# Performance work log

Hardware: AMD Instinct MI355X
Metric: run time of the kernel (lower is better)

Reference implementation:

```python
import jax, jax.numpy as jnp
from jax import lax
import numpy as np

DN = ('NDHWC', 'DHWIO', 'NDHWC')

def conv3d(x, w, b, stride=1):
    return lax.conv_general_dilated(x, w, (stride,) * 3, 'SAME', dimension_numbers=DN) + b

def convT3d(x, w, b, stride=2):
    return lax.conv_transpose(x, w, (stride,) * 3, 'SAME', dimension_numbers=DN) + b

def prelu(x, a):
    return jnp.where(x > 0, x, a * x)

def bn(x, g, be, m, v):
    # keras BatchNormalization, inference mode, epsilon=1e-3
    return (x - m) * g * lax.rsqrt(v + 1e-3) + be

def res_unit(x, c1w, c1b, c2w, c2b, g, be, m, v, a):
    # VQVAEResidualUnit: relu(x + PReLU(BN(conv2(swish(conv1(x))))))
    h = jax.nn.swish(conv3d(x, c1w, c1b))
    h = prelu(bn(conv3d(h, c2w, c2b), g, be, m, v), a)
    return jax.nn.relu(x + h)

def _forward(x, ec0_w, ec0_b, er0_c1w, er0_c1b, er0_c2w, er0_c2b, er0_g, er0_be, er0_m, er0_v, er0_a, ec1_w, ec1_b, er1_c1w, er1_c1b, er1_c2w, er1_c2b, er1_g, er1_be, er1_m, er1_v, er1_a, eo_w, eo_b, eo_a, codebook, dc0_w, dc0_b, dc0_a, dr0_c1w, dr0_c1b, dr0_c2w, dr0_c2b, dr0_g, dr0_be, dr0_m, dr0_v, dr0_a, du0_w, du0_b, dr1_c1w, dr1_c1b, dr1_c2w, dr1_c2b, dr1_g, dr1_be, dr1_m, dr1_v, dr1_a, du1_w, du1_b):
    # ----- Encoder -----
    h = jax.nn.relu(conv3d(x, ec0_w, ec0_b, stride=2))   # [B,64,64,64,64]
    h = res_unit(h, er0_c1w, er0_c1b, er0_c2w, er0_c2b, er0_g, er0_be, er0_m, er0_v, er0_a)
    h = jax.nn.relu(conv3d(h, ec1_w, ec1_b, stride=2))   # [B,32,32,32,128]
    h = res_unit(h, er1_c1w, er1_c1b, er1_c2w, er1_c2b, er1_g, er1_be, er1_m, er1_v, er1_a)
    z = prelu(conv3d(h, eo_w, eo_b), eo_a)               # [B,32,32,32,64] latent
    # ----- NSVQ (inference: hard codebook lookup) -----
    D = z.shape[-1]
    flat = z.reshape(-1, D)                              # [N, 64], N = B*32^3
    dist = (flat * flat).sum(1, keepdims=True) + (codebook * codebook).sum(1) - 2.0 * (flat @ codebook.T)  # [N, K]
    idx = jnp.argmin(dist, axis=1)
    zq = codebook[idx].reshape(z.shape)
    K = codebook.shape[0]
    p = jnp.zeros((K,), jnp.float32).at[idx].add(1.0) / flat.shape[0]
    perplexity = jnp.exp(-jnp.sum(p * jnp.log(p + 1e-12)))
    # ----- Decoder -----
    h = prelu(conv3d(zq, dc0_w, dc0_b), dc0_a)           # [B,32,32,32,128]
    h = res_unit(h, dr0_c1w, dr0_c1b, dr0_c2w, dr0_c2b, dr0_g, dr0_be, dr0_m, dr0_v, dr0_a)
    h = jax.nn.relu(convT3d(h, du0_w, du0_b))            # [B,64,64,64,64]
    h = res_unit(h, dr1_c1w, dr1_c1b, dr1_c2w, dr1_c2b, dr1_g, dr1_be, dr1_m, dr1_v, dr1_a)
    recon = convT3d(h, du1_w, du1_b)                     # [B,128,128,128,1]
    return recon, perplexity

def setup_inputs() -> dict:
    key = jax.random.key(0)
    ks = iter(jax.random.split(key, 40))
    nrm = lambda *s: jax.random.normal(next(ks), s, jnp.float32) * 0.05
    def ru(pfx, c):
        return {pfx + '_c1w': nrm(3, 3, 3, c, c), pfx + '_c1b': jnp.zeros((c,), jnp.float32),
                pfx + '_c2w': nrm(3, 3, 3, c, c), pfx + '_c2b': jnp.zeros((c,), jnp.float32),
                pfx + '_g': jnp.ones((c,), jnp.float32), pfx + '_be': jnp.zeros((c,), jnp.float32),
                pfx + '_m': jnp.zeros((c,), jnp.float32), pfx + '_v': jnp.ones((c,), jnp.float32),
                pfx + '_a': jnp.full((c,), 0.25, jnp.float32)}
    C0, C1, D, K = 64, 128, 64, 512
    inp = {'x': jax.random.normal(next(ks), (2, 128, 128, 128, 1), jnp.float32)}
    inp.update(ec0_w=nrm(4, 4, 4, 1, C0), ec0_b=jnp.zeros((C0,), jnp.float32))
    inp.update(ru('er0', C0))
    inp.update(ec1_w=nrm(4, 4, 4, C0, C1), ec1_b=jnp.zeros((C1,), jnp.float32))
    inp.update(ru('er1', C1))
    inp.update(eo_w=nrm(3, 3, 3, C1, D), eo_b=jnp.zeros((D,), jnp.float32), eo_a=jnp.full((D,), 0.25, jnp.float32))
    inp.update(codebook=jax.random.uniform(next(ks), (K, D), jnp.float32, -1.0, 1.0) * np.sqrt(6.0 / D).astype(np.float32))
    inp.update(dc0_w=nrm(3, 3, 3, D, C1), dc0_b=jnp.zeros((C1,), jnp.float32), dc0_a=jnp.full((C1,), 0.25, jnp.float32))
    inp.update(ru('dr0', C1))
    inp.update(du0_w=nrm(4, 4, 4, C1, C0), du0_b=jnp.zeros((C0,), jnp.float32))
    inp.update(ru('dr1', C0))
    inp.update(du1_w=nrm(4, 4, 4, C0, 1), du1_b=jnp.zeros((1,), jnp.float32))
    return inp

def reference(x, ec0_w, ec0_b, er0_c1w, er0_c1b, er0_c2w, er0_c2b, er0_g, er0_be, er0_m, er0_v, er0_a, ec1_w, ec1_b, er1_c1w, er1_c1b, er1_c2w, er1_c2b, er1_g, er1_be, er1_m, er1_v, er1_a, eo_w, eo_b, eo_a, codebook, dc0_w, dc0_b, dc0_a, dr0_c1w, dr0_c1b, dr0_c2w, dr0_c2b, dr0_g, dr0_be, dr0_m, dr0_v, dr0_a, du0_w, du0_b, dr1_c1w, dr1_c1b, dr1_c2w, dr1_c2b, dr1_g, dr1_be, dr1_m, dr1_v, dr1_a, du1_w, du1_b):
    return _forward(x, ec0_w, ec0_b, er0_c1w, er0_c1b, er0_c2w, er0_c2b, er0_g, er0_be, er0_m, er0_v, er0_a, ec1_w, ec1_b, er1_c1w, er1_c1b, er1_c2w, er1_c2b, er1_g, er1_be, er1_m, er1_v, er1_a, eo_w, eo_b, eo_a, codebook, dc0_w, dc0_b, dc0_a, dr0_c1w, dr0_c1b, dr0_c2w, dr0_c2b, dr0_g, dr0_be, dr0_m, dr0_v, dr0_a, du0_w, du0_b, dr1_c1w, dr1_c1b, dr1_c2w, dr1_c2b, dr1_g, dr1_be, dr1_m, dr1_v, dr1_a, du1_w, du1_b)
```

## Files before the change

### kernel.cpp

```cpp
#include <hip/hip_runtime.h>
#include <cstdint>


typedef unsigned short bf16_t;
typedef __attribute__((ext_vector_type(8)))  short s8b;
typedef __attribute__((ext_vector_type(16))) float f32x16;

__device__ __forceinline__ float b2f(bf16_t u) { return __uint_as_float((unsigned)u << 16); }
__device__ __forceinline__ bf16_t f2b(float f) {
    unsigned x = __float_as_uint(f);
    return (bf16_t)((x + 0x7FFFu + ((x >> 16) & 1u)) >> 16);
}

__device__ __forceinline__ void split3s(float v, unsigned short& h,
                                        unsigned short& m, unsigned short& l)
{
    const unsigned uv = __float_as_uint(v);
    const float fh = __uint_as_float(uv & 0xFFFF0000u);
    const float r1 = v - fh;
    const unsigned u1 = __float_as_uint(r1);
    const float fm = __uint_as_float(u1 & 0xFFFF0000u);
    const float r2 = r1 - fm;
    h = (unsigned short)(uv >> 16);
    m = (unsigned short)(u1 >> 16);
    l = (unsigned short)(__float_as_uint(r2) >> 16);
}

__device__ __forceinline__ int wdst(int tap, int ci_, int co_, int ci, int co)
{
    const int ks = ci_ >> 4, half = (ci_ >> 3) & 1, j = ci_ & 7;
    return (((tap * (ci >> 4) + ks) * 2 + half) * co + co_) * 8 + j;
}

__global__ __launch_bounds__(256)
void wprep3(const float* __restrict__ w, bf16_t* __restrict__ h,
            bf16_t* __restrict__ m, bf16_t* __restrict__ l,
            int ci, int co, int n)
{
    const int i = blockIdx.x * 256 + threadIdx.x;
    if (i >= n) return;
    const int co_ = i % co;
    const int ci_ = (i / co) % ci;
    const int tap = i / (co * ci);
    const int dst = wdst(tap, ci_, co_, ci, co);
    unsigned short hh, mm, ll2;
    split3s(w[i], hh, mm, ll2);
    h[dst] = hh; m[dst] = mm; l[dst] = ll2;
}

__global__ __launch_bounds__(256)
void wprep_split(const float* __restrict__ w, bf16_t* __restrict__ hi,
                 bf16_t* __restrict__ lo, int ci, int co, int n)
{
    const int i = blockIdx.x * 256 + threadIdx.x;
    if (i >= n) return;
    const int co_ = i % co;
    const int ci_ = (i / co) % ci;
    const int tap = i / (co * ci);
    const float v = w[i];
    const int dst = wdst(tap, ci_, co_, ci, co);
    const bf16_t h = f2b(v);
    hi[dst] = h;
    lo[dst] = f2b(v - b2f(h));
}

template<int CIN, int COUT, int SD, int NW, int EPI>
__global__ __launch_bounds__((SD / 32) * NW * 64)
void conv3e(const float* __restrict__ xf,
            const bf16_t* __restrict__ wh, const bf16_t* __restrict__ wm,
            const bf16_t* __restrict__ wl,
            const float* __restrict__ bias,
            const float* __restrict__ g, const float* __restrict__ be,
            const float* __restrict__ mn, const float* __restrict__ vr,
            const float* __restrict__ al,
            const float* skf, float* __restrict__ of)
{
    constexpr int NT = (SD / 32) * NW * 64;
    constexpr int LP = (SD * CIN) / (4 * NT);
    constexpr int KS = CIN / 16;
    __shared__ bf16_t lh[SD * CIN], lm[SD * CIN], ll[SD * CIN];

    const int tid  = threadIdx.x;
    const int lane = tid & 63;
    const int wid  = tid >> 6;
    const int wn   = wid % NW, wm2 = wid / NW;
    const int half = lane >> 5, ln = lane & 31;
    const int w    = wm2 * 32 + ln;
    const int nwg  = gridDim.x;
    const int bid  = (blockIdx.x & 7) * (nwg >> 3) + (blockIdx.x >> 3);
    const int h    = bid % SD;
    const int d    = (bid / SD) % SD;
    const int b    = bid / (SD * SD);
    const int cout0 = wn * 64 + ln;

    int pz[9], py[9], pt[9], np = 0;
    for (int kd = 0; kd < 3; ++kd) {
        const int iz = d + kd - 1;
        if ((unsigned)iz >= (unsigned)SD) continue;
        for (int kh = 0; kh < 3; ++kh) {
            const int iy = h + kh - 1;
            if ((unsigned)iy >= (unsigned)SD) continue;
            pz[np] = iz; py[np] = iy; pt[np] = (kd * 3 + kh) * 3; ++np;
        }
    }

    f32x16 accA[2], accB[2];
#pragma unroll
    for (int i = 0; i < 16; ++i) {
        accA[0][i] = 0.f; accA[1][i] = 0.f;
        accB[0][i] = 0.f; accB[1][i] = 0.f;
    }

    float4 rg[LP];
    auto loadrow = [&](int iz, int iy) {
        const float* src = xf + ((size_t)((b * SD + iz) * SD + iy)) * SD * CIN;
#pragma unroll
        for (int j = 0; j < LP; ++j)
            rg[j] = *reinterpret_cast<const float4*>(src + (size_t)(tid + j * NT) * 4);
    };
    auto writerow = [&]() {
#pragma unroll
        for (int j = 0; j < LP; ++j) {
            const int idx = (tid + j * NT) * 4;
            const int vox = idx / CIN, ch = idx % CIN;
            ushort4 h4, m4, l4;
            split3s(rg[j].x, h4.x, m4.x, l4.x);
            split3s(rg[j].y, h4.y, m4.y, l4.y);
            split3s(rg[j].z, h4.z, m4.z, l4.z);
            split3s(rg[j].w, h4.w, m4.w, l4.w);
            const int bo = ((vox * CIN + ch) * 2) ^ ((vox & 7) << 4);
            *reinterpret_cast<ushort4*>((char*)&lh[0] + bo) = h4;
            *reinterpret_cast<ushort4*>((char*)&lm[0] + bo) = m4;
            *reinterpret_cast<ushort4*>((char*)&ll[0] + bo) = l4;
        }
    };

    loadrow(pz[0], py[0]);
    writerow();
    __syncthreads();
#pragma unroll 1
    for (int i = 0; i < np; ++i) {
        if (i + 1 < np) loadrow(pz[i + 1], py[i + 1]);
#pragma unroll
        for (int kw = 0; kw < 3; ++kw) {
            const int tap = pt[i] + kw;
            const int iw = w + kw - 1;
            const bool edge = (unsigned)iw >= (unsigned)SD;
            const int wcl = edge ? w : iw;
            const s8b zz = {};
#pragma unroll
            for (int ks = 0; ks < KS; ++ks) {
                const int bo = ((wcl * CIN + half * 8 + ks * 16) * 2) ^ ((wcl & 7) << 4);
                s8b ah  = *reinterpret_cast<const s8b*>((const char*)&lh[0] + bo);
                s8b am  = *reinterpret_cast<const s8b*>((const char*)&lm[0] + bo);
                s8b al3 = *reinterpret_cast<const s8b*>((const char*)&ll[0] + bo);
                if (edge) { ah = zz; am = zz; al3 = zz; }
                const size_t wb0 = ((size_t)((tap * KS + ks) * 2 + half) * COUT + cout0) * 8;
#pragma unroll
                for (int n2 = 0; n2 < 2; ++n2) {
                    const size_t wb = wb0 + n2 * 256;
                    const s8b bh = *reinterpret_cast<const s8b*>(wh + wb);
                    const s8b bm = *reinterpret_cast<const s8b*>(wm + wb);
                    const s8b bl = *reinterpret_cast<const s8b*>(wl + wb);
                    accA[n2] = __builtin_amdgcn_mfma_f32_32x32x16_bf16(ah, bh, accA[n2], 0, 0, 0);
                    accB[n2] = __builtin_amdgcn_mfma_f32_32x32x16_bf16(ah, bm, accB[n2], 0, 0, 0);
                    accA[n2] = __builtin_amdgcn_mfma_f32_32x32x16_bf16(am, bh, accA[n2], 0, 0, 0);
                    accB[n2] = __builtin_amdgcn_mfma_f32_32x32x16_bf16(am, bm, accB[n2], 0, 0, 0);
                    accA[n2] = __builtin_amdgcn_mfma_f32_32x32x16_bf16(al3, bh, accA[n2], 0, 0, 0);
                    accB[n2] = __builtin_amdgcn_mfma_f32_32x32x16_bf16(ah, bl, accB[n2], 0, 0, 0);
                }
            }
        }
        if (i + 1 < np) {
            __syncthreads();
            writerow();
            __syncthreads();
        }
    }

    const size_t outrow = ((size_t)((b * SD + d) * SD + h)) * SD;
#pragma unroll
    for (int n2 = 0; n2 < 2; ++n2) {
        const int cout = wn * 64 + n2 * 32 + ln;
        const float bv = bias[cout];
        float sc = 0.f, mm = 0.f, bb2 = 0.f, aa = 0.f;
        if constexpr (EPI == 3) {
            sc = g[cout] * (1.0f / sqrtf(vr[cout] + 1e-3f));
            mm = mn[cout]; bb2 = be[cout]; aa = al[cout];
        }
        if constexpr (EPI == 2) aa = al[cout];
#pragma unroll
        for (int r = 0; r < 16; ++r) {
            const int rl = (r & 3) + 8 * (r >> 2) + 4 * half;
            const size_t oe = (outrow + wm2 * 32 + rl) * COUT + cout;
            float y = accA[n2][r] + accB[n2][r] + bv;
            if constexpr (EPI == 0) y = fmaxf(y, 0.f);
            else if constexpr (EPI == 1) y = y / (1.f + expf(-y));
            else if constexpr (EPI == 2) y = y > 0.f ? y : aa * y;
            else {
                float t2 = (y - mm) * sc + bb2;
                t2 = t2 > 0.f ? t2 : aa * t2;
                y = fmaxf(skf[oe] + t2, 0.f);
            }
            of[oe] = y;
        }
    }
}

__global__ __launch_bounds__(128)
void convs2e(const float* __restrict__ xf,
             const bf16_t* __restrict__ wh, const bf16_t* __restrict__ wm,
             const bf16_t* __restrict__ wl,
             const float* __restrict__ bias, float* __restrict__ of)
{
    constexpr int NT = 128, LP = (64 * 64) / (4 * NT);
    __shared__ bf16_t lh[64 * 64], lm[64 * 64], ll[64 * 64];

    const int tid  = threadIdx.x;
    const int lane = tid & 63;
    const int wn   = tid >> 6;
    const int half = lane >> 5, ln = lane & 31;
    const int nwg  = gridDim.x;
    const int bid  = (blockIdx.x & 7) * (nwg >> 3) + (blockIdx.x >> 3);
    const int h    = bid % 32;
    const int d    = (bid / 32) % 32;
    const int b    = bid / 1024;
    const int cout0 = wn * 64 + ln;

    int pz[16], py[16], pt[16], np = 0;
    for (int kd = 0; kd < 4; ++kd) {
        const int iz = 2 * d + kd - 1;
        if ((unsigned)iz >= 64u) continue;
        for (int kh = 0; kh < 4; ++kh) {
            const int iy = 2 * h + kh - 1;
            if ((unsigned)iy >= 64u) continue;
            pz[np] = iz; py[np] = iy; pt[np] = (kd * 4 + kh) * 4; ++np;
        }
    }

    f32x16 accA[2], accB[2];
#pragma unroll
    for (int i = 0; i < 16; ++i) {
        accA[0][i] = 0.f; accA[1][i] = 0.f;
        accB[0][i] = 0.f; accB[1][i] = 0.f;
    }

    float4 rg[LP];
    auto loadrow = [&](int iz, int iy) {
        const float* src = xf + ((size_t)((b * 64 + iz) * 64 + iy)) * 64 * 64;
#pragma unroll
        for (int j = 0; j < LP; ++j)
            rg[j] = *reinterpret_cast<const float4*>(src + (size_t)(tid + j * NT) * 4);
    };
    auto writerow = [&]() {
#pragma unroll
        for (int j = 0; j < LP; ++j) {
            const int idx = (tid + j * NT) * 4;
            const int vox = idx / 64, ch = idx % 64;
            ushort4 h4, m4, l4;
            split3s(rg[j].x, h4.x, m4.x, l4.x);
            split3s(rg[j].y, h4.y, m4.y, l4.y);
            split3s(rg[j].z, h4.z, m4.z, l4.z);
            split3s(rg[j].w, h4.w, m4.w, l4.w);
            const int bo = ((vox * 64 + ch) * 2) ^ ((vox & 7) << 4);
            *reinterpret_cast<ushort4*>((char*)&lh[0] + bo) = h4;
            *reinterpret_cast<ushort4*>((char*)&lm[0] + bo) = m4;
            *reinterpret_cast<ushort4*>((char*)&ll[0] + bo) = l4;
        }
    };

    loadrow(pz[0], py[0]);
    writerow();
    __syncthreads();
#pragma unroll 1
    for (int i = 0; i < np; ++i) {
        if (i + 1 < np) loadrow(pz[i + 1], py[i + 1]);
#pragma unroll
        for (int kw = 0; kw < 4; ++kw) {
            const int tap = pt[i] + kw;
            const int iw = 2 * ln + kw - 1;
            const bool edge = (unsigned)iw >= 64u;
            const int wcl = edge ? 2 * ln : iw;
            const s8b zz = {};
#pragma unroll
            for (int ks = 0; ks < 4; ++ks) {
                const int bo = ((wcl * 64 + half * 8 + ks * 16) * 2) ^ ((wcl & 7) << 4);
                s8b ah  = *reinterpret_cast<const s8b*>((const char*)&lh[0] + bo);
                s8b am  = *reinterpret_cast<const s8b*>((const char*)&lm[0] + bo);
                s8b al3 = *reinterpret_cast<const s8b*>((const char*)&ll[0] + bo);
                if (edge) { ah = zz; am = zz; al3 = zz; }
                const size_t wb0 = ((size_t)((tap * 4 + ks) * 2 + half) * 128 + cout0) * 8;
#pragma unroll
                for (int n2 = 0; n2 < 2; ++n2) {
                    const size_t wb = wb0 + n2 * 256;
                    const s8b bh = *reinterpret_cast<const s8b*>(wh + wb);
                    const s8b bm = *reinterpret_cast<const s8b*>(wm + wb);
                    const s8b bl = *reinterpret_cast<const s8b*>(wl + wb);
                    accA[n2] = __builtin_amdgcn_mfma_f32_32x32x16_bf16(ah, bh, accA[n2], 0, 0, 0);
                    accB[n2] = __builtin_amdgcn_mfma_f32_32x32x16_bf16(ah, bm, accB[n2], 0, 0, 0);
                    accA[n2] = __builtin_amdgcn_mfma_f32_32x32x16_bf16(am, bh, accA[n2], 0, 0, 0);
                    accB[n2] = __builtin_amdgcn_mfma_f32_32x32x16_bf16(am, bm, accB[n2], 0, 0, 0);
                    accA[n2] = __builtin_amdgcn_mfma_f32_32x32x16_bf16(al3, bh, accA[n2], 0, 0, 0);
                    accB[n2] = __builtin_amdgcn_mfma_f32_32x32x16_bf16(ah, bl, accB[n2], 0, 0, 0);
                }
            }
        }
        if (i + 1 < np) {
            __syncthreads();
            writerow();
            __syncthreads();
        }
    }

    const size_t outrow = ((size_t)((b * 32 + d) * 32 + h)) * 32;
#pragma unroll
    for (int n2 = 0; n2 < 2; ++n2) {
        const int cout = wn * 64 + n2 * 32 + ln;
        const float bv = bias[cout];
#pragma unroll
        for (int r = 0; r < 16; ++r) {
            const int rl = (r & 3) + 8 * (r >> 2) + 4 * half;
            const size_t oe = (outrow + rl) * 128 + cout;
            of[oe] = fmaxf(accA[n2][r] + accB[n2][r] + bv, 0.f);
        }
    }
}

template<int CIN, int COUT, int SD, int NW, int EPI>
__global__ __launch_bounds__((SD / 32) * NW * 64)
void conv3d(const bf16_t* __restrict__ xh, const bf16_t* __restrict__ xl,
            const bf16_t* __restrict__ wh, const bf16_t* __restrict__ wl,
            const float* __restrict__ bias,
            const float* __restrict__ g, const float* __restrict__ be,
            const float* __restrict__ mn, const float* __restrict__ vr,
            const float* __restrict__ al,
            const bf16_t* skh, const bf16_t* skl,
            bf16_t* oh, bf16_t* ol)
{
    constexpr int NT = (SD / 32) * NW * 64;
    constexpr int LP = (SD * CIN) / (4 * NT);
    constexpr int KS = CIN / 16;
    __shared__ bf16_t lh[SD * CIN], ll[SD * CIN];

    const int tid  = threadIdx.x;
    const int lane = tid & 63;
    const int wid  = tid >> 6;
    const int wn   = wid % NW, wm2 = wid / NW;
    const int half = lane >> 5, ln = lane & 31;
    const int w    = wm2 * 32 + ln;
    const int nwg  = gridDim.x;
    const int bid  = (blockIdx.x & 7) * (nwg >> 3) + (blockIdx.x >> 3);
    const int h    = bid % SD;
    const int d    = (bid / SD) % SD;
    const int b    = bid / (SD * SD);
    const int cout0 = wn * 64 + ln;

    int pz[9], py[9], pt[9], np = 0;
    for (int kd = 0; kd < 3; ++kd) {
        const int iz = d + kd - 1;
        if ((unsigned)iz >= (unsigned)SD) continue;
        for (int kh = 0; kh < 3; ++kh) {
            const int iy = h + kh - 1;
            if ((unsigned)iy >= (unsigned)SD) continue;
            pz[np] = iz; py[np] = iy; pt[np] = (kd * 3 + kh) * 3; ++np;
        }
    }

    f32x16 accA[2], accB[2];
#pragma unroll
    for (int i = 0; i < 16; ++i) {
        accA[0][i] = 0.f; accA[1][i] = 0.f;
        accB[0][i] = 0.f; accB[1][i] = 0.f;
    }

    ushort4 rh[LP], rl2[LP];
    auto loadrow = [&](int iz, int iy) {
        const size_t rb = ((size_t)((b * SD + iz) * SD + iy)) * SD * CIN;
#pragma unroll
        for (int j = 0; j < LP; ++j) {
            const int idx = (tid + j * NT) * 4;
            rh[j]  = *reinterpret_cast<const ushort4*>(xh + rb + idx);
            rl2[j] = *reinterpret_cast<const ushort4*>(xl + rb + idx);
        }
    };
    auto writerow = [&]() {
#pragma unroll
        for (int j = 0; j < LP; ++j) {
            const int idx = (tid + j * NT) * 4;
            const int vox = idx / CIN, ch = idx % CIN;
            const int bo = ((vox * CIN + ch) * 2) ^ ((vox & 7) << 4);
            *reinterpret_cast<ushort4*>((char*)&lh[0] + bo) = rh[j];
            *reinterpret_cast<ushort4*>((char*)&ll[0] + bo) = rl2[j];
        }
    };

    loadrow(pz[0], py[0]);
    writerow();
    __syncthreads();
#pragma unroll 1
    for (int i = 0; i < np; ++i) {
        if (i + 1 < np) loadrow(pz[i + 1], py[i + 1]);
#pragma unroll
        for (int kw = 0; kw < 3; ++kw) {
            const int tap = pt[i] + kw;
            const int iw = w + kw - 1;
            const bool edge = (unsigned)iw >= (unsigned)SD;
            const int wcl = edge ? w : iw;
            const s8b zz = {};
#pragma unroll
            for (int ks = 0; ks < KS; ++ks) {
                const int bo = ((wcl * CIN + half * 8 + ks * 16) * 2) ^ ((wcl & 7) << 4);
                s8b ah  = *reinterpret_cast<const s8b*>((const char*)&lh[0] + bo);
                s8b al2 = *reinterpret_cast<const s8b*>((const char*)&ll[0] + bo);
                if (edge) { ah = zz; al2 = zz; }
                const size_t wb0 = ((size_t)((tap * KS + ks) * 2 + half) * COUT + cout0) * 8;
#pragma unroll
                for (int n2 = 0; n2 < 2; ++n2) {
                    const size_t wb = wb0 + n2 * 256;
                    const s8b bh = *reinterpret_cast<const s8b*>(wh + wb);
                    const s8b bl = *reinterpret_cast<const s8b*>(wl + wb);
                    accA[n2] = __builtin_amdgcn_mfma_f32_32x32x16_bf16(ah, bh, accA[n2], 0, 0, 0);
                    accB[n2] = __builtin_amdgcn_mfma_f32_32x32x16_bf16(al2, bh, accB[n2], 0, 0, 0);
                    accB[n2] = __builtin_amdgcn_mfma_f32_32x32x16_bf16(ah, bl, accB[n2], 0, 0, 0);
                }
            }
        }
        if (i + 1 < np) {
            __syncthreads();
            writerow();
            __syncthreads();
        }
    }

    const size_t outrow = ((size_t)((b * SD + d) * SD + h)) * SD;
#pragma unroll
    for (int n2 = 0; n2 < 2; ++n2) {
        const int cout = wn * 64 + n2 * 32 + ln;
        const float bv = bias[cout];
        float sc = 0.f, mm = 0.f, bb2 = 0.f, aa = 0.f;
        if constexpr (EPI == 3) {
            sc = g[cout] * (1.0f / sqrtf(vr[cout] + 1e-3f));
            mm = mn[cout]; bb2 = be[cout]; aa = al[cout];
        }
        if constexpr (EPI == 2) aa = al[cout];
#pragma unroll
        for (int r = 0; r < 16; ++r) {
            const int rl = (r & 3) + 8 * (r >> 2) + 4 * half;
            const size_t oe = (outrow + wm2 * 32 + rl) * COUT + cout;
            float y = accA[n2][r] + accB[n2][r] + bv;
            if constexpr (EPI == 0) y = fmaxf(y, 0.f);
            else if constexpr (EPI == 1) y = y / (1.f + expf(-y));
            else if constexpr (EPI == 2) y = y > 0.f ? y : aa * y;
            else {
                float t2 = (y - mm) * sc + bb2;
                t2 = t2 > 0.f ? t2 : aa * t2;
                float sv = b2f(skh[oe]) + b2f(skl[oe]);
                y = fmaxf(sv + t2, 0.f);
            }
            const bf16_t hh = f2b(y);
            oh[oe] = hh;
            ol[oe] = f2b(y - b2f(hh));
        }
    }
}

__global__ __launch_bounds__(256)
void convTm(const bf16_t* __restrict__ xh, const bf16_t* __restrict__ xl,
            const bf16_t* __restrict__ wh, const bf16_t* __restrict__ wl,
            const float* __restrict__ bias,
            bf16_t* __restrict__ oh, bf16_t* __restrict__ ol)
{
    constexpr int NT = 256, LP = (32 * 128) / (4 * NT);
    __shared__ bf16_t lh[32 * 128], ll[32 * 128];

    const int tid  = threadIdx.x;
    const int lane = tid & 63;
    const int wid  = tid >> 6;
    const int wn   = wid & 1, p = wid >> 1;
    const int half = lane >> 5, ln = lane & 31;
    const int nwg  = gridDim.x;
    const int bid  = (blockIdx.x & 7) * (nwg >> 3) + (blockIdx.x >> 3);
    const int ohh  = bid % 64;
    const int od   = (bid / 64) % 64;
    const int b    = bid / 4096;
    const int pd = od & 1, dz = od >> 1;
    const int ph = ohh & 1, hy = ohh >> 1;
    const int cout = wn * 32 + ln;

    int pz[4], py[4], pt[4], np = 0;
    for (int jd = 0; jd < 2; ++jd) {
        const int kd = pd + 2 * jd;
        const int iz = dz + pd - 1 + jd;
        if ((unsigned)iz >= 32u) continue;
        for (int jh = 0; jh < 2; ++jh) {
            const int kh = ph + 2 * jh;
            const int iy = hy + ph - 1 + jh;
            if ((unsigned)iy >= 32u) continue;
            pz[np] = iz; py[np] = iy; pt[np] = (kd * 4 + kh) * 4; ++np;
        }
    }

    f32x16 accA, accB;
#pragma unroll
    for (int i = 0; i < 16; ++i) { accA[i] = 0.0f; accB[i] = 0.0f; }

    ushort4 rh[LP], rl2[LP];
    auto loadrow = [&](int iz, int iy) {
        const size_t rb = ((size_t)((b * 32 + iz) * 32 + iy)) * 32 * 128;
#pragma unroll
        for (int j = 0; j < LP; ++j) {
            const int idx = (tid + j * NT) * 4;
            rh[j]  = *reinterpret_cast<const ushort4*>(xh + rb + idx);
            rl2[j] = *reinterpret_cast<const ushort4*>(xl + rb + idx);
        }
    };
    auto writerow = [&]() {
#pragma unroll
        for (int j = 0; j < LP; ++j) {
            const int idx = (tid + j * NT) * 4;
            const int vox = idx / 128, ch = idx % 128;
            const int bo = ((vox * 128 + ch) * 2) ^ ((vox & 7) << 4);
            *reinterpret_cast<ushort4*>((char*)&lh[0] + bo) = rh[j];
            *reinterpret_cast<ushort4*>((char*)&ll[0] + bo) = rl2[j];
        }
    };

    loadrow(pz[0], py[0]);
    writerow();
    __syncthreads();
#pragma unroll 1
    for (int i = 0; i < np; ++i) {
        if (i + 1 < np) loadrow(pz[i + 1], py[i + 1]);
#pragma unroll
        for (int jw = 0; jw < 2; ++jw) {
            const int kw = p + 2 * jw;
            const int tap = pt[i] + kw;
            const int ix = ln + p - 1 + jw;
            const bool edge = (unsigned)ix >= 32u;
            const int xcl = edge ? ln : ix;
            const s8b zz = {};
#pragma unroll
            for (int ks = 0; ks < 8; ++ks) {
                const int bo = ((xcl * 128 + half * 8 + ks * 16) * 2) ^ ((xcl & 7) << 4);
                s8b a  = *reinterpret_cast<const s8b*>((const char*)&lh[0] + bo);
                s8b a2 = *reinterpret_cast<const s8b*>((const char*)&ll[0] + bo);
                if (edge) { a = zz; a2 = zz; }
                const size_t wb = ((size_t)((tap * 8 + ks) * 2 + half) * 64 + cout) * 8;
                const s8b bb = *reinterpret_cast<const s8b*>(wh + wb);
                const s8b b2 = *reinterpret_cast<const s8b*>(wl + wb);
                accA = __builtin_amdgcn_mfma_f32_32x32x16_bf16(a, bb, accA, 0, 0, 0);
                accB = __builtin_amdgcn_mfma_f32_32x32x16_bf16(a2, bb, accB, 0, 0, 0);
                accB = __builtin_amdgcn_mfma_f32_32x32x16_bf16(a, b2, accB, 0, 0, 0);
            }
        }
        if (i + 1 < np) {
            __syncthreads();
            writerow();
            __syncthreads();
        }
    }

    const float bv = bias[cout];
#pragma unroll
    for (int r = 0; r < 16; ++r) {
        const int rl = (r & 3) + 8 * (r >> 2) + 4 * half;
        const int ow = 2 * rl + p;
        const size_t oe = (((size_t)((b * 64 + od) * 64 + ohh)) * 64 + ow) * 64 + cout;
        const float y = fmaxf(accA[r] + accB[r] + bv, 0.f);
        const bf16_t hh = f2b(y);
        oh[oe] = hh;
        ol[oe] = f2b(y - b2f(hh));
    }
}

__global__ __launch_bounds__(128)
void conv_ec0m(const float* __restrict__ x,
               const bf16_t* __restrict__ wh, const bf16_t* __restrict__ wm,
               const bf16_t* __restrict__ wl,
               const float* __restrict__ bias, float* __restrict__ of)
{
    __shared__ bf16_t lh[16 * 132], lm[16 * 132], ll[16 * 132];

    const int tid  = threadIdx.x;
    const int lane = tid & 63;
    const int wm2  = tid >> 6;
    const int half = lane >> 5, ln = lane & 31;
    const int w    = wm2 * 32 + ln;
    const int nwg  = gridDim.x;
    const int bid  = (blockIdx.x & 7) * (nwg >> 3) + (blockIdx.x >> 3);
    const int h    = bid % 64;
    const int d    = (bid / 64) % 64;
    const int b    = bid / 4096;

    for (int i = tid; i < 16 * 132; i += 128) {
        const int row = i / 132, col = i % 132;
        const int kd = row >> 2, kh = row & 3;
        const int iz = 2 * d + kd - 1, iy = 2 * h + kh - 1;
        const int ix = col - 1;
        float v = 0.f;
        if ((unsigned)iz < 128u && (unsigned)iy < 128u &&
            (unsigned)ix < 128u && col < 130)
            v = x[(size_t)((b * 128 + iz) * 128 + iy) * 128 + ix];
        unsigned short hh, mm2, ll2;
        split3s(v, hh, mm2, ll2);
        lh[i] = hh; lm[i] = mm2; ll[i] = ll2;
    }
    __syncthreads();

    f32x16 accA[2], accB[2];
#pragma unroll
    for (int i = 0; i < 16; ++i) {
        accA[0][i] = 0.f; accA[1][i] = 0.f;
        accB[0][i] = 0.f; accB[1][i] = 0.f;
    }

#pragma unroll
    for (int ks = 0; ks < 4; ++ks) {
        const int row0 = ks * 4 + 2 * half;
        const int i0 = row0 * 132 + 2 * w;
        const int i1 = i0 + 132;
        s8b ah, am, al3;
        {
            uint* ap = (uint*)&ah;
            ap[0] = *(const uint*)&lh[i0]; ap[1] = *(const uint*)&lh[i0 + 2];
            ap[2] = *(const uint*)&lh[i1]; ap[3] = *(const uint*)&lh[i1 + 2];
        }
        {
            uint* ap = (uint*)&am;
            ap[0] = *(const uint*)&lm[i0]; ap[1] = *(const uint*)&lm[i0 + 2];
            ap[2] = *(const uint*)&lm[i1]; ap[3] = *(const uint*)&lm[i1 + 2];
        }
        {
            uint* ap = (uint*)&al3;
            ap[0] = *(const uint*)&ll[i0]; ap[1] = *(const uint*)&ll[i0 + 2];
            ap[2] = *(const uint*)&ll[i1]; ap[3] = *(const uint*)&ll[i1 + 2];
        }
        const size_t wb0 = ((size_t)(ks * 2 + half) * 64 + ln) * 8;
#pragma unroll
        for (int n2 = 0; n2 < 2; ++n2) {
            const size_t wb = wb0 + n2 * 256;
            const s8b bh = *reinterpret_cast<const s8b*>(wh + wb);
            const s8b bm = *reinterpret_cast<const s8b*>(wm + wb);
            const s8b bl = *reinterpret_cast<const s8b*>(wl + wb);
            accA[n2] = __builtin_amdgcn_mfma_f32_32x32x16_bf16(ah, bh, accA[n2], 0, 0, 0);
            accB[n2] = __builtin_amdgcn_mfma_f32_32x32x16_bf16(ah, bm, accB[n2], 0, 0, 0);
            accA[n2] = __builtin_amdgcn_mfma_f32_32x32x16_bf16(am, bh, accA[n2], 0, 0, 0);
            accB[n2] = __builtin_amdgcn_mfma_f32_32x32x16_bf16(am, bm, accB[n2], 0, 0, 0);
            accA[n2] = __builtin_amdgcn_mfma_f32_32x32x16_bf16(al3, bh, accA[n2], 0, 0, 0);
            accB[n2] = __builtin_amdgcn_mfma_f32_32x32x16_bf16(ah, bl, accB[n2], 0, 0, 0);
        }
    }

    const size_t outrow = ((size_t)((b * 64 + d) * 64 + h)) * 64;
#pragma unroll
    for (int n2 = 0; n2 < 2; ++n2) {
        const int cout = n2 * 32 + ln;
        const float bv = bias[cout];
#pragma unroll
        for (int r = 0; r < 16; ++r) {
            const int rl = (r & 3) + 8 * (r >> 2) + 4 * half;
            const size_t oe = (outrow + wm2 * 32 + rl) * 64 + cout;
            of[oe] = fmaxf(accA[n2][r] + accB[n2][r] + bv, 0.f);
        }
    }
}

__global__ __launch_bounds__(256)
void convT_du1w(const bf16_t* __restrict__ inh, const bf16_t* __restrict__ inl,
                const float* __restrict__ wt, const float* __restrict__ bias,
                float* __restrict__ out)
{
    const int lane = threadIdx.x & 63;
    const int wv   = blockIdx.x * 4 + (threadIdx.x >> 6);
    const size_t obase = (size_t)wv * 16;
    const int ow0 = (int)(obase % 128);
    size_t rem = obase / 128;
    const int ohh = (int)(rem % 128); rem /= 128;
    const int od  = (int)(rem % 128); rem /= 128;
    const int b   = (int)rem;
    const int pd = od & 1, dz = od >> 1;
    const int ph = ohh & 1, hy = ohh >> 1;
    const int wx0 = ow0 >> 1;

    float acc[16];
#pragma unroll
    for (int o = 0; o < 16; ++o) acc[o] = 0.f;

#pragma unroll
    for (int jd = 0; jd < 2; ++jd) {
        const int kd = pd + 2 * jd;
        const int iz = dz + pd - 1 + jd;
        if ((unsigned)iz >= 64u) continue;
#pragma unroll
        for (int jh = 0; jh < 2; ++jh) {
            const int kh = ph + 2 * jh;
            const int iy = hy + ph - 1 + jh;
            if ((unsigned)iy >= 64u) continue;
            const size_t rbase = ((size_t)((b * 64 + iz) * 64 + iy)) * 64;
            float wv4[4];
#pragma unroll
            for (int kw = 0; kw < 4; ++kw)
                wv4[kw] = wt[(size_t)((kd * 4 + kh) * 4 + kw) * 64 + lane];
            float v[10];
#pragma unroll
            for (int t = 0; t < 10; ++t) {
                const int ix = wx0 - 1 + t;
                if ((unsigned)ix < 64u) {
                    const size_t a = (rbase + ix) * 64 + lane;
                    v[t] = b2f(inh[a]) + b2f(inl[a]);
                } else {
                    v[t] = 0.f;
                }
            }
#pragma unroll
            for (int o = 0; o < 16; ++o) {
// ... 103 lines not shown
    const float* er0_c1w = (const float*)d_in[3];
    const float* er0_c1b = (const float*)d_in[4];
    const float* er0_c2w = (const float*)d_in[5];
    const float* er0_c2b = (const float*)d_in[6];
    const float* er0_g   = (const float*)d_in[7];
    const float* er0_be  = (const float*)d_in[8];
    const float* er0_m   = (const float*)d_in[9];
    const float* er0_v   = (const float*)d_in[10];
    const float* er0_a   = (const float*)d_in[11];
    const float* ec1_w   = (const float*)d_in[12];
    const float* ec1_b   = (const float*)d_in[13];
    const float* er1_c1w = (const float*)d_in[14];
    const float* er1_c1b = (const float*)d_in[15];
    const float* er1_c2w = (const float*)d_in[16];
    const float* er1_c2b = (const float*)d_in[17];
    const float* er1_g   = (const float*)d_in[18];
    const float* er1_be  = (const float*)d_in[19];
    const float* er1_m   = (const float*)d_in[20];
    const float* er1_v   = (const float*)d_in[21];
    const float* er1_a   = (const float*)d_in[22];
    const float* eo_w    = (const float*)d_in[23];
    const float* eo_b    = (const float*)d_in[24];
    const float* eo_a    = (const float*)d_in[25];
    const float* cb      = (const float*)d_in[26];
    const float* dc0_w   = (const float*)d_in[27];
    const float* dc0_b   = (const float*)d_in[28];
    const float* dc0_a   = (const float*)d_in[29];
    const float* dr0_c1w = (const float*)d_in[30];
    const float* dr0_c1b = (const float*)d_in[31];
    const float* dr0_c2w = (const float*)d_in[32];
    const float* dr0_c2b = (const float*)d_in[33];
    const float* dr0_g   = (const float*)d_in[34];
    const float* dr0_be  = (const float*)d_in[35];
    const float* dr0_m   = (const float*)d_in[36];
    const float* dr0_v   = (const float*)d_in[37];
    const float* dr0_a   = (const float*)d_in[38];
    const float* du0_w   = (const float*)d_in[39];
    const float* du0_b   = (const float*)d_in[40];
    const float* dr1_c1w = (const float*)d_in[41];
    const float* dr1_c1b = (const float*)d_in[42];
    const float* dr1_c2w = (const float*)d_in[43];
    const float* dr1_c2b = (const float*)d_in[44];
    const float* dr1_g   = (const float*)d_in[45];
    const float* dr1_be  = (const float*)d_in[46];
    const float* dr1_m   = (const float*)d_in[47];
    const float* dr1_v   = (const float*)d_in[48];
    const float* dr1_a   = (const float*)d_in[49];
    const float* du1_w   = (const float*)d_in[50];
    const float* du1_b   = (const float*)d_in[51];

    float* out = (float*)d_out;

    char* W = (char*)d_ws;
    float*  Af  = (float*)(W);
    float*  Hf  = (float*)(W + 134217728);
    float*  E1f = (float*)(W + 134217728);
    float*  R1f = (float*)(W + 134217728 + 33554432);
    float*  Zf  = (float*)(W);
    int*    IDX = (int*)  (W + 16777216);
    float*  CN  = (float*)(W + 17039360);
    float*  HS  = (float*)(W + 17041408);
    bf16_t* ZQh = (bf16_t*)(W + 33554432);
    bf16_t* ZQl = (bf16_t*)(W + 41943040);
    bf16_t* D0h = (bf16_t*)(W + 50331648);
    bf16_t* D0l = (bf16_t*)(W + 67108864);
    bf16_t* Gh  = (bf16_t*)(W + 83886080);
    bf16_t* Gl  = (bf16_t*)(W + 100663296);
    bf16_t* U0h = (bf16_t*)(W + 134217728);
    bf16_t* U0l = (bf16_t*)(W + 201326592);
    bf16_t* G1h = (bf16_t*)(W);
    bf16_t* G1l = (bf16_t*)(W + 67108864);

    char* WB = (char*)d_out;
    bf16_t* e0c1h = (bf16_t*)(WB + 0);
    bf16_t* e0c1m = (bf16_t*)(WB + 221184);
    bf16_t* e0c1l = (bf16_t*)(WB + 442368);
    bf16_t* e0c2h = (bf16_t*)(WB + 663552);
    bf16_t* e0c2m = (bf16_t*)(WB + 884736);
    bf16_t* e0c2l = (bf16_t*)(WB + 1105920);
    bf16_t* ec1h  = (bf16_t*)(WB + 1327104);
    bf16_t* ec1m  = (bf16_t*)(WB + 2375680);
    bf16_t* ec1l  = (bf16_t*)(WB + 3424256);
    bf16_t* e1c1h = (bf16_t*)(WB + 4472832);
    bf16_t* e1c1m = (bf16_t*)(WB + 5357568);
    bf16_t* e1c1l = (bf16_t*)(WB + 6242304);
    bf16_t* e1c2h = (bf16_t*)(WB + 7127040);
    bf16_t* e1c2m = (bf16_t*)(WB + 8011776);
    bf16_t* e1c2l = (bf16_t*)(WB + 8896512);
    bf16_t* eoh   = (bf16_t*)(WB + 9781248);
    bf16_t* eom   = (bf16_t*)(WB + 10223616);
    bf16_t* eol   = (bf16_t*)(WB + 10665984);
    bf16_t* wec0h = (bf16_t*)(WB + 11108352);
    bf16_t* wec0m = (bf16_t*)(WB + 11116544);
    bf16_t* wec0l = (bf16_t*)(WB + 11124736);
    bf16_t* dc0h  = (bf16_t*)(WB + 0);
    bf16_t* dc0l  = (bf16_t*)(WB + 442368);
    bf16_t* d0c1h = (bf16_t*)(WB + 884736);
    bf16_t* d0c1l = (bf16_t*)(WB + 1769472);
    bf16_t* d0c2h = (bf16_t*)(WB + 2654208);
    bf16_t* d0c2l = (bf16_t*)(WB + 3538944);
    bf16_t* du0h  = (bf16_t*)(WB + 4423680);
    bf16_t* du0l  = (bf16_t*)(WB + 5472256);
    bf16_t* d1c1h = (bf16_t*)(WB + 6520832);
    bf16_t* d1c1l = (bf16_t*)(WB + 6742016);
    bf16_t* d1c2h = (bf16_t*)(WB + 6963200);
    bf16_t* d1c2l = (bf16_t*)(WB + 7184384);

    const float* fn = nullptr;
    const bf16_t* bn_ = nullptr;

    wprep3<<<16, 256, 0, stream>>>(ec0_w, wec0h, wec0m, wec0l, 64, 64, 4096);
    wprep3<<<432, 256, 0, stream>>>(er0_c1w, e0c1h, e0c1m, e0c1l, 64, 64, 110592);
    wprep3<<<432, 256, 0, stream>>>(er0_c2w, e0c2h, e0c2m, e0c2l, 64, 64, 110592);
    wprep3<<<2048, 256, 0, stream>>>(ec1_w, ec1h, ec1m, ec1l, 64, 128, 524288);
    wprep3<<<1728, 256, 0, stream>>>(er1_c1w, e1c1h, e1c1m, e1c1l, 128, 128, 442368);
    wprep3<<<1728, 256, 0, stream>>>(er1_c2w, e1c2h, e1c2m, e1c2l, 128, 128, 442368);
    wprep3<<<864, 256, 0, stream>>>(eo_w, eoh, eom, eol, 128, 64, 221184);

    conv_ec0m<<<8192, 128, 0, stream>>>(x, wec0h, wec0m, wec0l, ec0_b, Af);

    conv3e<64, 64, 64, 1, 1><<<8192, 128, 0, stream>>>(
        Af, e0c1h, e0c1m, e0c1l, er0_c1b, fn, fn, fn, fn, fn, fn, Hf);
    conv3e<64, 64, 64, 1, 3><<<8192, 128, 0, stream>>>(
        Hf, e0c2h, e0c2m, e0c2l, er0_c2b, er0_g, er0_be, er0_m, er0_v, er0_a, Af, Af);

    convs2e<<<2048, 128, 0, stream>>>(Af, ec1h, ec1m, ec1l, ec1_b, E1f);

    conv3e<128, 128, 32, 2, 1><<<2048, 128, 0, stream>>>(
        E1f, e1c1h, e1c1m, e1c1l, er1_c1b, fn, fn, fn, fn, fn, fn, R1f);
    conv3e<128, 128, 32, 2, 3><<<2048, 128, 0, stream>>>(
        R1f, e1c2h, e1c2m, e1c2l, er1_c2b, er1_g, er1_be, er1_m, er1_v, er1_a, E1f, E1f);

    conv3e<128, 64, 32, 1, 2><<<2048, 64, 0, stream>>>(
        E1f, eoh, eom, eol, eo_b, fn, fn, fn, fn, eo_a, fn, Zf);

    vq_cnorm<<<8, 64, 0, stream>>>(cb, CN);
    zero512<<<1, 512, 0, stream>>>(HS);
    vq_assign<<<256, 256, 0, stream>>>(Zf, cb, CN, IDX, HS, 65536);
    perplexity_k<<<1, 512, 0, stream>>>(HS, out + 4194304, 1.0f / 65536.0f);
    vq_gather_split<<<4096, 256, 0, stream>>>(cb, IDX, ZQh, ZQl);

    wprep_split<<<864, 256, 0, stream>>>(dc0_w, dc0h, dc0l, 64, 128, 221184);
    wprep_split<<<1728, 256, 0, stream>>>(dr0_c1w, d0c1h, d0c1l, 128, 128, 442368);
    wprep_split<<<1728, 256, 0, stream>>>(dr0_c2w, d0c2h, d0c2l, 128, 128, 442368);
    wprep_split<<<2048, 256, 0, stream>>>(du0_w, du0h, du0l, 128, 64, 524288);
    wprep_split<<<432, 256, 0, stream>>>(dr1_c1w, d1c1h, d1c1l, 64, 64, 110592);
    wprep_split<<<432, 256, 0, stream>>>(dr1_c2w, d1c2h, d1c2l, 64, 64, 110592);

    conv3d<64, 128, 32, 2, 2><<<2048, 128, 0, stream>>>(
        ZQh, ZQl, dc0h, dc0l, dc0_b, fn, fn, fn, fn, dc0_a, bn_, bn_, D0h, D0l);
    conv3d<128, 128, 32, 2, 1><<<2048, 128, 0, stream>>>(
        D0h, D0l, d0c1h, d0c1l, dr0_c1b, fn, fn, fn, fn, fn, bn_, bn_, Gh, Gl);
    conv3d<128, 128, 32, 2, 3><<<2048, 128, 0, stream>>>(
        Gh, Gl, d0c2h, d0c2l, dr0_c2b, dr0_g, dr0_be, dr0_m, dr0_v, dr0_a,
        D0h, D0l, D0h, D0l);

    convTm<<<8192, 256, 0, stream>>>(D0h, D0l, du0h, du0l, du0_b, U0h, U0l);

    conv3d<64, 64, 64, 1, 1><<<8192, 128, 0, stream>>>(
        U0h, U0l, d1c1h, d1c1l, dr1_c1b, fn, fn, fn, fn, fn, bn_, bn_, G1h, G1l);
    conv3d<64, 64, 64, 1, 3><<<8192, 128, 0, stream>>>(
        G1h, G1l, d1c2h, d1c2l, dr1_c2b, dr1_g, dr1_be, dr1_m, dr1_v, dr1_a,
        U0h, U0l, U0h, U0l);

    convT_du1w<<<65536, 256, 0, stream>>>(U0h, U0l, du1_w, du1_b, out);
}
```

Measured before the change: 5.506 ms.

## Store encoder activations pre-split as three bf16 planes instead of fp32

Encoder kernels (first conv, residual convs, stride-2 conv) now write their outputs already split into hi/mid/lo bf16 planes. Consumers copy those planes straight into shared memory instead of re-running the three-way split on every row load, and each row is loaded for several taps. The residual epilogue rebuilds the skip value from the three planes. Activation storage grows from 4 to 6 bytes per element, so global traffic rises. To fit the workspace, the full-resolution encoder stage now runs as a loop over the two batch samples, which doubles its kernel launches.

```diff
diff --git a/kernel.cpp b/kernel.cpp
--- a/kernel.cpp
+++ b/kernel.cpp
@@ -64,16 +64,18 @@
     lo[dst] = f2b(v - b2f(h));
 }
 
-template<int CIN, int COUT, int SD, int NW, int EPI>
+template<int CIN, int COUT, int SD, int NW, int EPI, int OM>
 __global__ __launch_bounds__((SD / 32) * NW * 64)
-void conv3e(const float* __restrict__ xf,
+void conv3e(const bf16_t* __restrict__ xh, const bf16_t* __restrict__ xm,
+            const bf16_t* __restrict__ xl,
             const bf16_t* __restrict__ wh, const bf16_t* __restrict__ wm,
             const bf16_t* __restrict__ wl,
             const float* __restrict__ bias,
             const float* __restrict__ g, const float* __restrict__ be,
             const float* __restrict__ mn, const float* __restrict__ vr,
             const float* __restrict__ al,
-            const float* skf, float* __restrict__ of)
+            const bf16_t* sh, const bf16_t* sm, const bf16_t* sl,
+            bf16_t* oh, bf16_t* om_, bf16_t* ol_, float* of)
 {
     constexpr int NT = (SD / 32) * NW * 64;
     constexpr int LP = (SD * CIN) / (4 * NT);
@@ -111,27 +113,26 @@
         accB[0][i] = 0.f; accB[1][i] = 0.f;
     }
 
-    float4 rg[LP];
+    ushort4 rh[LP], rm[LP], rl[LP];
     auto loadrow = [&](int iz, int iy) {
-        const float* src = xf + ((size_t)((b * SD + iz) * SD + iy)) * SD * CIN;
-#pragma unroll
-        for (int j = 0; j < LP; ++j)
-            rg[j] = *reinterpret_cast<const float4*>(src + (size_t)(tid + j * NT) * 4);
+        const size_t rb = ((size_t)((b * SD + iz) * SD + iy)) * SD * CIN;
+#pragma unroll
+        for (int j = 0; j < LP; ++j) {
+            const int idx = (tid + j * NT) * 4;
+            rh[j] = *reinterpret_cast<const ushort4*>(xh + rb + idx);
+            rm[j] = *reinterpret_cast<const ushort4*>(xm + rb + idx);
+            rl[j] = *reinterpret_cast<const ushort4*>(xl + rb + idx);
+        }
     };
     auto writerow = [&]() {
 #pragma unroll
         for (int j = 0; j < LP; ++j) {
             const int idx = (tid + j * NT) * 4;
             const int vox = idx / CIN, ch = idx % CIN;
-            ushort4 h4, m4, l4;
-            split3s(rg[j].x, h4.x, m4.x, l4.x);
-            split3s(rg[j].y, h4.y, m4.y, l4.y);
-            split3s(rg[j].z, h4.z, m4.z, l4.z);
-            split3s(rg[j].w, h4.w, m4.w, l4.w);
             const int bo = ((vox * CIN + ch) * 2) ^ ((vox & 7) << 4);
-            *reinterpret_cast<ushort4*>((char*)&lh[0] + bo) = h4;
-            *reinterpret_cast<ushort4*>((char*)&lm[0] + bo) = m4;
-            *reinterpret_cast<ushort4*>((char*)&ll[0] + bo) = l4;
+            *reinterpret_cast<ushort4*>((char*)&lh[0] + bo) = rh[j];
+            *reinterpret_cast<ushort4*>((char*)&lm[0] + bo) = rm[j];
+            *reinterpret_cast<ushort4*>((char*)&ll[0] + bo) = rl[j];
         }
     };
 
@@ -191,8 +192,8 @@
         if constexpr (EPI == 2) aa = al[cout];
 #pragma unroll
         for (int r = 0; r < 16; ++r) {
-            const int rl = (r & 3) + 8 * (r >> 2) + 4 * half;
-            const size_t oe = (outrow + wm2 * 32 + rl) * COUT + cout;
+            const int rl2 = (r & 3) + 8 * (r >> 2) + 4 * half;
+            const size_t oe = (outrow + wm2 * 32 + rl2) * COUT + cout;
             float y = accA[n2][r] + accB[n2][r] + bv;
             if constexpr (EPI == 0) y = fmaxf(y, 0.f);
             else if constexpr (EPI == 1) y = y / (1.f + expf(-y));
@@ -200,18 +201,28 @@
             else {
                 float t2 = (y - mm) * sc + bb2;
                 t2 = t2 > 0.f ? t2 : aa * t2;
-                y = fmaxf(skf[oe] + t2, 0.f);
+                const float sv = b2f(sh[oe]) + b2f(sm[oe]) + b2f(sl[oe]);
+                y = fmaxf(sv + t2, 0.f);
             }
-            of[oe] = y;
+            if constexpr (OM == 1) {
+                of[oe] = y;
+            } else {
+                unsigned short yh, ym, yl;
+                split3s(y, yh, ym, yl);
+                oh[oe] = yh; om_[oe] = ym; ol_[oe] = yl;
+            }
         }
     }
 }
 
 __global__ __launch_bounds__(128)
-void convs2e(const float* __restrict__ xf,
+void convs2e(const bf16_t* __restrict__ xh, const bf16_t* __restrict__ xm,
+             const bf16_t* __restrict__ xl,
              const bf16_t* __restrict__ wh, const bf16_t* __restrict__ wm,
              const bf16_t* __restrict__ wl,
-             const float* __restrict__ bias, float* __restrict__ of)
+             const float* __restrict__ bias,
+             bf16_t* __restrict__ oh, bf16_t* __restrict__ om_,
+             bf16_t* __restrict__ ol_)
 {
     constexpr int NT = 128, LP = (64 * 64) / (4 * NT);
     __shared__ bf16_t lh[64 * 64], lm[64 * 64], ll[64 * 64];
@@ -245,27 +256,26 @@
         accB[0][i] = 0.f; accB[1][i] = 0.f;
     }
 
-    float4 rg[LP];
+    ushort4 rh[LP], rm[LP], rl[LP];
     auto loadrow = [&](int iz, int iy) {
-        const float* src = xf + ((size_t)((b * 64 + iz) * 64 + iy)) * 64 * 64;
-#pragma unroll
-        for (int j = 0; j < LP; ++j)
-            rg[j] = *reinterpret_cast<const float4*>(src + (size_t)(tid + j * NT) * 4);
+        const size_t rb = ((size_t)((b * 64 + iz) * 64 + iy)) * 64 * 64;
+#pragma unroll
+        for (int j = 0; j < LP; ++j) {
+            const int idx = (tid + j * NT) * 4;
+            rh[j] = *reinterpret_cast<const ushort4*>(xh + rb + idx);
+            rm[j] = *reinterpret_cast<const ushort4*>(xm + rb + idx);
+            rl[j] = *reinterpret_cast<const ushort4*>(xl + rb + idx);
+        }
     };
     auto writerow = [&]() {
 #pragma unroll
         for (int j = 0; j < LP; ++j) {
             const int idx = (tid + j * NT) * 4;
             const int vox = idx / 64, ch = idx % 64;
-            ushort4 h4, m4, l4;
-            split3s(rg[j].x, h4.x, m4.x, l4.x);
-            split3s(rg[j].y, h4.y, m4.y, l4.y);
-            split3s(rg[j].z, h4.z, m4.z, l4.z);
-            split3s(rg[j].w, h4.w, m4.w, l4.w);
             const int bo = ((vox * 64 + ch) * 2) ^ ((vox & 7) << 4);
-            *reinterpret_cast<ushort4*>((char*)&lh[0] + bo) = h4;
-            *reinterpret_cast<ushort4*>((char*)&lm[0] + bo) = m4;
-            *reinterpret_cast<ushort4*>((char*)&ll[0] + bo) = l4;
+            *reinterpret_cast<ushort4*>((char*)&lh[0] + bo) = rh[j];
+            *reinterpret_cast<ushort4*>((char*)&lm[0] + bo) = rm[j];
+            *reinterpret_cast<ushort4*>((char*)&ll[0] + bo) = rl[j];
         }
     };
 
@@ -319,9 +329,12 @@
         const float bv = bias[cout];
 #pragma unroll
         for (int r = 0; r < 16; ++r) {
-            const int rl = (r & 3) + 8 * (r >> 2) + 4 * half;
-            const size_t oe = (outrow + rl) * 128 + cout;
-            of[oe] = fmaxf(accA[n2][r] + accB[n2][r] + bv, 0.f);
+            const int rl2 = (r & 3) + 8 * (r >> 2) + 4 * half;
+            const size_t oe = (outrow + rl2) * 128 + cout;
+            const float y = fmaxf(accA[n2][r] + accB[n2][r] + bv, 0.f);
+            unsigned short yh, ym, yl;
+            split3s(y, yh, ym, yl);
+            oh[oe] = yh; om_[oe] = ym; ol_[oe] = yl;
         }
     }
 }
@@ -373,14 +386,14 @@
         accB[0][i] = 0.f; accB[1][i] = 0.f;
     }
 
-    ushort4 rh[LP], rl2[LP];
+    ushort4 rh[LP], rl2a[LP];
     auto loadrow = [&](int iz, int iy) {
         const size_t rb = ((size_t)((b * SD + iz) * SD + iy)) * SD * CIN;
 #pragma unroll
         for (int j = 0; j < LP; ++j) {
             const int idx = (tid + j * NT) * 4;
-            rh[j]  = *reinterpret_cast<const ushort4*>(xh + rb + idx);
-            rl2[j] = *reinterpret_cast<const ushort4*>(xl + rb + idx);
+            rh[j]   = *reinterpret_cast<const ushort4*>(xh + rb + idx);
+            rl2a[j] = *reinterpret_cast<const ushort4*>(xl + rb + idx);
         }
     };
     auto writerow = [&]() {
@@ -390,7 +403,7 @@
             const int vox = idx / CIN, ch = idx % CIN;
             const int bo = ((vox * CIN + ch) * 2) ^ ((vox & 7) << 4);
             *reinterpret_cast<ushort4*>((char*)&lh[0] + bo) = rh[j];
-            *reinterpret_cast<ushort4*>((char*)&ll[0] + bo) = rl2[j];
+            *reinterpret_cast<ushort4*>((char*)&ll[0] + bo) = rl2a[j];
         }
     };
 
@@ -445,8 +458,8 @@
         if constexpr (EPI == 2) aa = al[cout];
 #pragma unroll
         for (int r = 0; r < 16; ++r) {
-            const int rl = (r & 3) + 8 * (r >> 2) + 4 * half;
-            const size_t oe = (outrow + wm2 * 32 + rl) * COUT + cout;
+            const int rl3 = (r & 3) + 8 * (r >> 2) + 4 * half;
+            const size_t oe = (outrow + wm2 * 32 + rl3) * COUT + cout;
             float y = accA[n2][r] + accB[n2][r] + bv;
             if constexpr (EPI == 0) y = fmaxf(y, 0.f);
             else if constexpr (EPI == 1) y = y / (1.f + expf(-y));
@@ -504,14 +517,14 @@
 #pragma unroll
     for (int i = 0; i < 16; ++i) { accA[i] = 0.0f; accB[i] = 0.0f; }
 
-    ushort4 rh[LP], rl2[LP];
+    ushort4 rh[LP], rl2a[LP];
     auto loadrow = [&](int iz, int iy) {
         const size_t rb = ((size_t)((b * 32 + iz) * 32 + iy)) * 32 * 128;
 #pragma unroll
         for (int j = 0; j < LP; ++j) {
             const int idx = (tid + j * NT) * 4;
-            rh[j]  = *reinterpret_cast<const ushort4*>(xh + rb + idx);
-            rl2[j] = *reinterpret_cast<const ushort4*>(xl + rb + idx);
+            rh[j]   = *reinterpret_cast<const ushort4*>(xh + rb + idx);
+            rl2a[j] = *reinterpret_cast<const ushort4*>(xl + rb + idx);
         }
     };
     auto writerow = [&]() {
@@ -521,7 +534,7 @@
             const int vox = idx / 128, ch = idx % 128;
             const int bo = ((vox * 128 + ch) * 2) ^ ((vox & 7) << 4);
             *reinterpret_cast<ushort4*>((char*)&lh[0] + bo) = rh[j];
-            *reinterpret_cast<ushort4*>((char*)&ll[0] + bo) = rl2[j];
+            *reinterpret_cast<ushort4*>((char*)&ll[0] + bo) = rl2a[j];
         }
     };
 
@@ -563,8 +576,8 @@
     const float bv = bias[cout];
 #pragma unroll
     for (int r = 0; r < 16; ++r) {
-        const int rl = (r & 3) + 8 * (r >> 2) + 4 * half;
-        const int ow = 2 * rl + p;
+        const int rl3 = (r & 3) + 8 * (r >> 2) + 4 * half;
+        const int ow = 2 * rl3 + p;
         const size_t oe = (((size_t)((b * 64 + od) * 64 + ohh)) * 64 + ow) * 64 + cout;
         const float y = fmaxf(accA[r] + accB[r] + bv, 0.f);
         const bf16_t hh = f2b(y);
@@ -577,7 +590,9 @@
 void conv_ec0m(const float* __restrict__ x,
                const bf16_t* __restrict__ wh, const bf16_t* __restrict__ wm,
                const bf16_t* __restrict__ wl,
-               const float* __restrict__ bias, float* __restrict__ of)
+               const float* __restrict__ bias,
+               bf16_t* __restrict__ oh, bf16_t* __restrict__ om_,
+               bf16_t* __restrict__ ol_)
 {
     __shared__ bf16_t lh[16 * 132], lm[16 * 132], ll[16 * 132];
 
@@ -658,9 +673,12 @@
         const float bv = bias[cout];
 #pragma unroll
         for (int r = 0; r < 16; ++r) {
-            const int rl = (r & 3) + 8 * (r >> 2) + 4 * half;
-            const size_t oe = (outrow + wm2 * 32 + rl) * 64 + cout;
-            of[oe] = fmaxf(accA[n2][r] + accB[n2][r] + bv, 0.f);
+            const int rl3 = (r & 3) + 8 * (r >> 2) + 4 * half;
+            const size_t oe = (outrow + wm2 * 32 + rl3) * 64 + cout;
+            const float y = fmaxf(accA[n2][r] + accB[n2][r] + bv, 0.f);
+            unsigned short yh, ym, yl;
+            split3s(y, yh, ym, yl);
+            oh[oe] = yh; om_[oe] = ym; ol_[oe] = yl;
         }
     }
 }
@@ -870,14 +888,22 @@
     float* out = (float*)d_out;
 
     char* W = (char*)d_ws;
-    float*  Af  = (float*)(W);
-    float*  Hf  = (float*)(W + 134217728);
-    float*  E1f = (float*)(W + 134217728);
-    float*  R1f = (float*)(W + 134217728 + 33554432);
-    float*  Zf  = (float*)(W);
-    int*    IDX = (int*)  (W + 16777216);
-    float*  CN  = (float*)(W + 17039360);
-    float*  HS  = (float*)(W + 17041408);
+    bf16_t* Ah = (bf16_t*)(W);
+    bf16_t* Am = (bf16_t*)(W + 33554432);
+    bf16_t* Al = (bf16_t*)(W + 67108864);
+    bf16_t* Hh = (bf16_t*)(W + 100663296);
+    bf16_t* Hm = (bf16_t*)(W + 134217728);
+    bf16_t* Hl = (bf16_t*)(W + 167772160);
+    bf16_t* E1h = (bf16_t*)(W + 201326592);
+    bf16_t* E1m = (bf16_t*)(W + 218103808);
+    bf16_t* E1l = (bf16_t*)(W + 234881024);
+    bf16_t* R1h = (bf16_t*)(W + 100663296);
+    bf16_t* R1m = (bf16_t*)(W + 117440512);
+    bf16_t* R1l = (bf16_t*)(W + 134217728);
+    float*  Zf  = (float*) (W);
+    int*    IDX = (int*)   (W + 16777216);
+    float*  CN  = (float*) (W + 17039360);
+    float*  HS  = (float*) (W + 17041408);
     bf16_t* ZQh = (bf16_t*)(W + 33554432);
     bf16_t* ZQl = (bf16_t*)(W + 41943040);
     bf16_t* D0h = (bf16_t*)(W + 50331648);
@@ -926,6 +952,7 @@
 
     const float* fn = nullptr;
     const bf16_t* bn_ = nullptr;
+    bf16_t* bo = nullptr;
 
     wprep3<<<16, 256, 0, stream>>>(ec0_w, wec0h, wec0m, wec0l, 64, 64, 4096);
     wprep3<<<432, 256, 0, stream>>>(er0_c1w, e0c1h, e0c1m, e0c1l, 64, 64, 110592);
@@ -935,22 +962,34 @@
     wprep3<<<1728, 256, 0, stream>>>(er1_c2w, e1c2h, e1c2m, e1c2l, 128, 128, 442368);
     wprep3<<<864, 256, 0, stream>>>(eo_w, eoh, eom, eol, 128, 64, 221184);
 
-    conv_ec0m<<<8192, 128, 0, stream>>>(x, wec0h, wec0m, wec0l, ec0_b, Af);
-
-    conv3e<64, 64, 64, 1, 1><<<8192, 128, 0, stream>>>(
-        Af, e0c1h, e0c1m, e0c1l, er0_c1b, fn, fn, fn, fn, fn, fn, Hf);
-    conv3e<64, 64, 64, 1, 3><<<8192, 128, 0, stream>>>(
-        Hf, e0c2h, e0c2m, e0c2l, er0_c2b, er0_g, er0_be, er0_m, er0_v, er0_a, Af, Af);
-
-    convs2e<<<2048, 128, 0, stream>>>(Af, ec1h, ec1m, ec1l, ec1_b, E1f);
-
-    conv3e<128, 128, 32, 2, 1><<<2048, 128, 0, stream>>>(
-        E1f, e1c1h, e1c1m, e1c1l, er1_c1b, fn, fn, fn, fn, fn, fn, R1f);
-    conv3e<128, 128, 32, 2, 3><<<2048, 128, 0, stream>>>(
-        R1f, e1c2h, e1c2m, e1c2l, er1_c2b, er1_g, er1_be, er1_m, er1_v, er1_a, E1f, E1f);
-
-    conv3e<128, 64, 32, 1, 2><<<2048, 64, 0, stream>>>(
-        E1f, eoh, eom, eol, eo_b, fn, fn, fn, fn, eo_a, fn, Zf);
+    for (int b = 0; b < 2; ++b) {
+        const float* xb = x + (size_t)b * 2097152;
+        bf16_t* E1hb = E1h + (size_t)b * 4194304;
+        bf16_t* E1mb = E1m + (size_t)b * 4194304;
+        bf16_t* E1lb = E1l + (size_t)b * 4194304;
+
+        conv_ec0m<<<4096, 128, 0, stream>>>(xb, wec0h, wec0m, wec0l, ec0_b,
+                                            Ah, Am, Al);
+        conv3e<64, 64, 64, 1, 1, 0><<<4096, 128, 0, stream>>>(
+            Ah, Am, Al, e0c1h, e0c1m, e0c1l, er0_c1b, fn, fn, fn, fn, fn,
+            bn_, bn_, bn_, Hh, Hm, Hl, nullptr);
+        conv3e<64, 64, 64, 1, 3, 0><<<4096, 128, 0, stream>>>(
+            Hh, Hm, Hl, e0c2h, e0c2m, e0c2l, er0_c2b, er0_g, er0_be, er0_m,
+            er0_v, er0_a, Ah, Am, Al, Ah, Am, Al, nullptr);
+        convs2e<<<1024, 128, 0, stream>>>(Ah, Am, Al, ec1h, ec1m, ec1l, ec1_b,
+                                          E1hb, E1mb, E1lb);
+    }
+
+    conv3e<128, 128, 32, 2, 1, 0><<<2048, 128, 0, stream>>>(
+        E1h, E1m, E1l, e1c1h, e1c1m, e1c1l, er1_c1b, fn, fn, fn, fn, fn,
+        bn_, bn_, bn_, R1h, R1m, R1l, nullptr);
+    conv3e<128, 128, 32, 2, 3, 0><<<2048, 128, 0, stream>>>(
+        R1h, R1m, R1l, e1c2h, e1c2m, e1c2l, er1_c2b, er1_g, er1_be, er1_m, er1_v, er1_a,
+        E1h, E1m, E1l, E1h, E1m, E1l, nullptr);
+
+    conv3e<128, 64, 32, 1, 2, 1><<<2048, 64, 0, stream>>>(
+        E1h, E1m, E1l, eoh, eom, eol, eo_b, fn, fn, fn, fn, eo_a,
+        bn_, bn_, bn_, bo, bo, bo, Zf);
 
     vq_cnorm<<<8, 64, 0, stream>>>(cb, CN);
     zero512<<<1, 512, 0, stream>>>(HS);
```

Measured after the change: 6.105 ms. 10.9% more time.
